# Optimization experiments

Hardware: AMD Instinct MI355X
Metric: run time of the kernel (lower is better)

## Reference

```python
import jax, jax.numpy as jnp
import numpy as np
from math import sqrt

N, D = 8192, 64

def setup_inputs() -> dict:
    key = jax.random.key(0)
    kq, kk, kv = jax.random.split(key, 3)
    q = jax.random.normal(kq, (N, D), dtype=jnp.float32)
    k = jax.random.normal(kk, (N, D), dtype=jnp.float32)
    v = jax.random.normal(kv, (N, D), dtype=jnp.float32)
    return {"q": q, "k": k, "v": v}

def reference(q, k, v):
    # Mathematically identical to the block-wise online-softmax loop:
    # after processing all KV blocks, m_blk == rowmax(S), l_blk == rowsum(exp(S - m)),
    # O = (exp(S - m) @ V) / l.
    scale = 1.0 / sqrt(q.shape[-1])
    S = (q @ k.T) * scale            # [N, N] attention scores
    m = jnp.max(S, axis=1, keepdims=True)   # running max -> global row max
    P = jnp.exp(S - m)                      # unnormalized probs
    L = jnp.sum(P, axis=1, keepdims=True)   # softmax denominator, [N, 1]
    O = (P @ v) / L                          # [N, D]
    return (O, L)
```

## Files before the change

kernel.cpp:

```cpp
#include <hip/hip_runtime.h>
#include <hip/hip_bf16.h>
#include <math.h>

#define N 8192
#define D 64
#define QSCALE 0.18033688011112042f

typedef __attribute__((ext_vector_type(8))) short short8;
typedef __attribute__((ext_vector_type(16))) float f32x16;
typedef __attribute__((ext_vector_type(4))) unsigned int ui4;

__device__ inline short f32_to_bf16_bits(float x) {
    unsigned u = __builtin_bit_cast(unsigned, x);
    u += 0x7FFFu + ((u >> 16) & 1u);
    return (short)(u >> 16);
}
__device__ inline float bfbits_to_f32(unsigned short u) {
    return __builtin_bit_cast(float, ((unsigned)u) << 16);
}
__device__ inline unsigned cvt_pk_bf16(float a, float b) {
    unsigned r;
    asm("v_cvt_pk_bf16_f32 %0, %1, %2" : "=v"(r) : "v"(a), "v"(b));
    return r;
}
__device__ inline float max3f(float a, float b, float c) {
    float d;
    asm("v_max3_f32 %0, %1, %2, %3" : "=v"(d) : "v"(a), "v"(b), "v"(c));
    return d;
}

__global__ __launch_bounds__(256) void fa_conv(const float* __restrict__ q,
                                               const float* __restrict__ k,
                                               const float* __restrict__ v,
                                               short* __restrict__ Qb,
                                               short* __restrict__ Kp,
                                               short* __restrict__ Vp) {
    int bid = blockIdx.x, tid = threadIdx.x;
    if (bid < 512) {
        int i = (bid * 256 + tid) * 4;
        float4 a = *(const float4*)(q + i);
        unsigned lo = cvt_pk_bf16(a.x * QSCALE, a.y * QSCALE);
        unsigned hi = cvt_pk_bf16(a.z * QSCALE, a.w * QSCALE);
        unsigned long long u = (unsigned long long)lo | ((unsigned long long)hi << 32);
        *(unsigned long long*)(Qb + i) = u;
    } else if (bid < 768) {
        int t = bid - 512;
        int c = tid >> 6, l = tid & 63, ql = l & 31, hi = l >> 5;
        const float* src = k + (size_t)(t * 32 + ql) * D + c * 16 + hi * 8;
        float4 a = *(const float4*)(src);
        float4 b = *(const float4*)(src + 4);
        uint4 u = { cvt_pk_bf16(a.x, a.y), cvt_pk_bf16(a.z, a.w),
                    cvt_pk_bf16(b.x, b.y), cvt_pk_bf16(b.z, b.w) };
        *(uint4*)(Kp + (size_t)t * 2048 + c * 512 + l * 8) = u;
    } else {
        int t = bid - 768;
        int dt = tid >> 7, h = (tid >> 6) & 1, hi = (tid >> 5) & 1, ql = tid & 31;
        const float* src = v + (size_t)(t * 32 + h * 16 + hi * 4) * D + dt * 32 + ql;
        float f[8];
#pragma unroll
        for (int j = 0; j < 8; ++j)
            f[j] = src[(size_t)((j & 3) + 8 * (j >> 2)) * D];
        uint4 u = { cvt_pk_bf16(f[0], f[1]), cvt_pk_bf16(f[2], f[3]),
                    cvt_pk_bf16(f[4], f[5]), cvt_pk_bf16(f[6], f[7]) };
        *(uint4*)(Vp + (size_t)t * 2048 + dt * 1024 + h * 512 + hi * 256 + ql * 8) = u;
    }
}

__global__ __launch_bounds__(256) void fa_part_kernel(const short* __restrict__ Qb,
                                                      const short* __restrict__ Kp,
                                                      const short* __restrict__ Vp,
                                                      short* __restrict__ OTb,
                                                      float* __restrict__ Ml,
                                                      int KN) {
    const int s  = blockIdx.x & 15;
    const int qt = blockIdx.x >> 4;
    const int w = threadIdx.x >> 6, lane = threadIdx.x & 63;
    const int ql = lane & 31, hi = lane >> 5;
    const int qrow = qt * 128 + w * 32 + ql;

    const short* qp = Qb + (size_t)qrow * D + hi * 8;
    short8 qf0 = *(const short8*)(qp);
    short8 qf1 = *(const short8*)(qp + 16);
    short8 qf2 = *(const short8*)(qp + 32);
    short8 qf3 = *(const short8*)(qp + 48);

    f32x16 acc0 = {}, acc1 = {};
    float mex = -INFINITY, lsum = 0.f;

    const int t0 = (s * KN) >> 5, nt = KN >> 5;
    const short* kp = Kp + (size_t)t0 * 2048 + lane * 8;
    const short* vp = Vp + (size_t)t0 * 2048 + lane * 8;

    short8 kA0, kA1, kA2, kA3, kB0, kB1, kB2, kB3;
    short8 vA0, vA1, vA2, vA3, vB0, vB1, vB2, vB3;

#define LOADK(d0, d1, d2, d3) do {                                         \
        d0 = *(const short8*)(kp);                                         \
        d1 = *(const short8*)(kp + 512);                                   \
        d2 = *(const short8*)(kp + 1024);                                  \
        d3 = *(const short8*)(kp + 1536);                                  \
        kp += 2048;                                                        \
    } while (0)
#define LOADV(d0, d1, d2, d3) do {                                         \
        d0 = *(const short8*)(vp);                                         \
        d1 = *(const short8*)(vp + 512);                                   \
        d2 = *(const short8*)(vp + 1024);                                  \
        d3 = *(const short8*)(vp + 1536);                                  \
        vp += 2048;                                                        \
    } while (0)

#define TILE(K0, K1, K2, K3, V0, V1, V2, V3) do {                           \
        f32x16 st = {};                                                     \
        st = __builtin_amdgcn_mfma_f32_32x32x16_bf16(K0, qf0, st, 0, 0, 0); \
        st = __builtin_amdgcn_mfma_f32_32x32x16_bf16(K1, qf1, st, 0, 0, 0); \
        st = __builtin_amdgcn_mfma_f32_32x32x16_bf16(K2, qf2, st, 0, 0, 0); \
        st = __builtin_amdgcn_mfma_f32_32x32x16_bf16(K3, qf3, st, 0, 0, 0); \
        float m0_ = max3f(st[0], st[1], st[2]);                             \
        float m1_ = max3f(st[3], st[4], st[5]);                             \
        float m2_ = max3f(st[6], st[7], st[8]);                             \
        float m3_ = max3f(st[9], st[10], st[11]);                           \
        float m4_ = max3f(st[12], st[13], st[14]);                          \
        mex = max3f(mex, max3f(m0_, m1_, m2_), max3f(m3_, m4_, st[15]));    \
        unsigned pk0, pk1, pk2, pk3, pk4, pk5, pk6, pk7;                    \
        float rs_;                                                          \
        {                                                                   \
            float a_, b_;                                                   \
            a_ = __builtin_amdgcn_exp2f(st[0]);  b_ = __builtin_amdgcn_exp2f(st[1]);  \
            rs_ = a_ + b_;         pk0 = cvt_pk_bf16(a_, b_);               \
            a_ = __builtin_amdgcn_exp2f(st[2]);  b_ = __builtin_amdgcn_exp2f(st[3]);  \
            rs_ += a_ + b_;        pk1 = cvt_pk_bf16(a_, b_);               \
            a_ = __builtin_amdgcn_exp2f(st[4]);  b_ = __builtin_amdgcn_exp2f(st[5]);  \
            rs_ += a_ + b_;        pk2 = cvt_pk_bf16(a_, b_);               \
            a_ = __builtin_amdgcn_exp2f(st[6]);  b_ = __builtin_amdgcn_exp2f(st[7]);  \
            rs_ += a_ + b_;        pk3 = cvt_pk_bf16(a_, b_);               \
            a_ = __builtin_amdgcn_exp2f(st[8]);  b_ = __builtin_amdgcn_exp2f(st[9]);  \
            rs_ += a_ + b_;        pk4 = cvt_pk_bf16(a_, b_);               \
            a_ = __builtin_amdgcn_exp2f(st[10]); b_ = __builtin_amdgcn_exp2f(st[11]); \
            rs_ += a_ + b_;        pk5 = cvt_pk_bf16(a_, b_);               \
            a_ = __builtin_amdgcn_exp2f(st[12]); b_ = __builtin_amdgcn_exp2f(st[13]); \
            rs_ += a_ + b_;        pk6 = cvt_pk_bf16(a_, b_);               \
            a_ = __builtin_amdgcn_exp2f(st[14]); b_ = __builtin_amdgcn_exp2f(st[15]); \
            rs_ += a_ + b_;        pk7 = cvt_pk_bf16(a_, b_);               \
        }                                                                   \
        lsum += rs_;                                                        \
        ui4 va_ = { pk0, pk1, pk2, pk3 };                                   \
        ui4 vb_ = { pk4, pk5, pk6, pk7 };                                   \
        short8 pb0 = __builtin_bit_cast(short8, va_);                       \
        short8 pb1 = __builtin_bit_cast(short8, vb_);                       \
        acc0 = __builtin_amdgcn_mfma_f32_32x32x16_bf16(V0, pb0, acc0, 0, 0, 0); \
        acc0 = __builtin_amdgcn_mfma_f32_32x32x16_bf16(V1, pb1, acc0, 0, 0, 0); \
        acc1 = __builtin_amdgcn_mfma_f32_32x32x16_bf16(V2, pb0, acc1, 0, 0, 0); \
        acc1 = __builtin_amdgcn_mfma_f32_32x32x16_bf16(V3, pb1, acc1, 0, 0, 0); \
    } while (0)

    LOADK(kA0, kA1, kA2, kA3);
    LOADV(vA0, vA1, vA2, vA3);
#pragma unroll 1
    for (int T = 0; T < nt; T += 2) {
        LOADK(kB0, kB1, kB2, kB3);
        LOADV(vB0, vB1, vB2, vB3);
        TILE(kA0, kA1, kA2, kA3, vA0, vA1, vA2, vA3);
        if (T + 2 < nt) {
            LOADK(kA0, kA1, kA2, kA3);
            LOADV(vA0, vA1, vA2, vA3);
        }
        TILE(kB0, kB1, kB2, kB3, vB0, vB1, vB2, vB3);
    }
#undef LOADK
#undef LOADV
#undef TILE

    mex = fmaxf(mex, __shfl_xor(mex, 32));
    lsum += __shfl_xor(lsum, 32);

#pragma unroll
    for (int r = 0; r < 16; ++r) {
        int d0 = (r & 3) + 8 * (r >> 2) + 4 * hi;
        OTb[(size_t)(s * 64 + d0) * N + qrow]      = f32_to_bf16_bits(acc0[r]);
        OTb[(size_t)(s * 64 + 32 + d0) * N + qrow] = f32_to_bf16_bits(acc1[r]);
    }
    if (hi == 0) {
        Ml[(size_t)(s * 2 + 0) * N + qrow] = lsum;
        Ml[(size_t)(s * 2 + 1) * N + qrow] = mex;
    }
}

__global__ __launch_bounds__(256) void fa_comb_kernel(const short* __restrict__ OTb,
                                                      const float* __restrict__ Ml,
                                                      float* __restrict__ Out, int S) {
    const int qb = blockIdx.x >> 2, db4 = blockIdx.x & 3;
    const int row = threadIdx.x & 63, dd = threadIdx.x >> 6;
    const int grow = qb * 64 + row;
    const int d0 = db4 * 16 + dd * 4;

    float v0 = 0.f, v1 = 0.f, v2 = 0.f, v3 = 0.f;
    float L = 0.f, mg = -INFINITY;
    for (int s = 0; s < S; ++s) {
        size_t base = (size_t)(s * 64 + d0) * N + grow;
        v0 += bfbits_to_f32((unsigned short)OTb[base]);
        v1 += bfbits_to_f32((unsigned short)OTb[base + (size_t)N]);
        v2 += bfbits_to_f32((unsigned short)OTb[base + (size_t)2 * N]);
        v3 += bfbits_to_f32((unsigned short)OTb[base + (size_t)3 * N]);
        L  += Ml[(size_t)(s * 2 + 0) * N + grow];
        mg = fmaxf(mg, Ml[(size_t)(s * 2 + 1) * N + grow]);
    }
    float inv = 1.0f / L;
    float4 o = { v0 * inv, v1 * inv, v2 * inv, v3 * inv };
    *(float4*)(Out + (size_t)grow * D + d0) = o;
    if (db4 == 0 && dd == 0) Out[(size_t)N * D + grow] = exp2f(-mg) * L;
}

extern "C" void kernel_launch(void* const* d_in, const int* in_sizes, int n_in,
                              void* d_out, int out_size, void* d_ws, size_t ws_size,
                              hipStream_t stream) {
    const float* q = (const float*)d_in[0];
    const float* k = (const float*)d_in[1];
    const float* v = (const float*)d_in[2];
    float* out = (float*)d_out;

    short* Qb = (short*)d_ws;
    short* Kp = Qb + (size_t)N * D;
    short* Vp = Kp + (size_t)N * D;
    short* OTb = (short*)((char*)d_ws + 3 * 1048576);

    int S = 16;
    while (S > 1 &&
           3ull * 1048576 + (size_t)S * (64ull * N * 2) + (size_t)S * (2ull * N * 4) > ws_size)
        S >>= 1;
    float* Ml = (float*)(OTb + (size_t)S * 64 * N);
    int KN = N / S;

    fa_conv<<<1024, 256, 0, stream>>>(q, k, v, Qb, Kp, Vp);
    fa_part_kernel<<<64 * S, 256, 0, stream>>>(Qb, Kp, Vp, OTb, Ml, KN);
    fa_comb_kernel<<<(N / 64) * 4, 256, 0, stream>>>(OTb, Ml, out, S);
}
```

Baseline: 45.36 us.

## Fuse bf16 conversion into attention kernel, stage K/V in LDS, use 32 splits

```diff
diff --git a/kernel.cpp b/kernel.cpp
--- a/kernel.cpp
+++ b/kernel.cpp
@@ -5,6 +5,9 @@
 #define N 8192
 #define D 64
 #define QSCALE 0.18033688011112042f
+#define SPLITS 32
+#define KVS 256
+#define NT (KVS / 32)
 
 typedef __attribute__((ext_vector_type(8))) short short8;
 typedef __attribute__((ext_vector_type(16))) float f32x16;
@@ -29,67 +32,75 @@
     return d;
 }
 
-__global__ __launch_bounds__(256) void fa_conv(const float* __restrict__ q,
-                                               const float* __restrict__ k,
-                                               const float* __restrict__ v,
-                                               short* __restrict__ Qb,
-                                               short* __restrict__ Kp,
-                                               short* __restrict__ Vp) {
-    int bid = blockIdx.x, tid = threadIdx.x;
-    if (bid < 512) {
-        int i = (bid * 256 + tid) * 4;
-        float4 a = *(const float4*)(q + i);
-        unsigned lo = cvt_pk_bf16(a.x * QSCALE, a.y * QSCALE);
-        unsigned hi = cvt_pk_bf16(a.z * QSCALE, a.w * QSCALE);
-        unsigned long long u = (unsigned long long)lo | ((unsigned long long)hi << 32);
-        *(unsigned long long*)(Qb + i) = u;
-    } else if (bid < 768) {
-        int t = bid - 512;
-        int c = tid >> 6, l = tid & 63, ql = l & 31, hi = l >> 5;
-        const float* src = k + (size_t)(t * 32 + ql) * D + c * 16 + hi * 8;
-        float4 a = *(const float4*)(src);
-        float4 b = *(const float4*)(src + 4);
-        uint4 u = { cvt_pk_bf16(a.x, a.y), cvt_pk_bf16(a.z, a.w),
-                    cvt_pk_bf16(b.x, b.y), cvt_pk_bf16(b.z, b.w) };
-        *(uint4*)(Kp + (size_t)t * 2048 + c * 512 + l * 8) = u;
-    } else {
-        int t = bid - 768;
-        int dt = tid >> 7, h = (tid >> 6) & 1, hi = (tid >> 5) & 1, ql = tid & 31;
-        const float* src = v + (size_t)(t * 32 + h * 16 + hi * 4) * D + dt * 32 + ql;
-        float f[8];
-#pragma unroll
-        for (int j = 0; j < 8; ++j)
-            f[j] = src[(size_t)((j & 3) + 8 * (j >> 2)) * D];
-        uint4 u = { cvt_pk_bf16(f[0], f[1]), cvt_pk_bf16(f[2], f[3]),
-                    cvt_pk_bf16(f[4], f[5]), cvt_pk_bf16(f[6], f[7]) };
-        *(uint4*)(Vp + (size_t)t * 2048 + dt * 1024 + h * 512 + hi * 256 + ql * 8) = u;
-    }
-}
-
-__global__ __launch_bounds__(256) void fa_part_kernel(const short* __restrict__ Qb,
-                                                      const short* __restrict__ Kp,
-                                                      const short* __restrict__ Vp,
+__global__ __launch_bounds__(256) void fa_part_kernel(const float* __restrict__ q,
+                                                      const float* __restrict__ k,
+                                                      const float* __restrict__ v,
                                                       short* __restrict__ OTb,
-                                                      float* __restrict__ Ml,
-                                                      int KN) {
-    const int s  = blockIdx.x & 15;
-    const int qt = blockIdx.x >> 4;
-    const int w = threadIdx.x >> 6, lane = threadIdx.x & 63;
+                                                      float* __restrict__ Ml) {
+    __shared__ short Klds[KVS * D];
+    __shared__ short Vlds[KVS * D];
+
+    const int s  = blockIdx.x & 31;
+    const int qt = blockIdx.x >> 5;
+    const int tid = threadIdx.x;
+    const int w = tid >> 6, lane = tid & 63;
     const int ql = lane & 31, hi = lane >> 5;
     const int qrow = qt * 128 + w * 32 + ql;
-
-    const short* qp = Qb + (size_t)qrow * D + hi * 8;
-    short8 qf0 = *(const short8*)(qp);
-    short8 qf1 = *(const short8*)(qp + 16);
-    short8 qf2 = *(const short8*)(qp + 32);
-    short8 qf3 = *(const short8*)(qp + 48);
+    const int k0 = s * KVS;
+
+    {
+        const int c = tid >> 6, l = tid & 63, kq = l & 31, kh = l >> 5;
+#pragma unroll
+        for (int t = 0; t < NT; ++t) {
+            const float* src = k + (size_t)(k0 + t * 32 + kq) * D + c * 16 + kh * 8;
+            float4 a = *(const float4*)(src);
+            float4 b = *(const float4*)(src + 4);
+            ui4 u = { cvt_pk_bf16(a.x, a.y), cvt_pk_bf16(a.z, a.w),
+                      cvt_pk_bf16(b.x, b.y), cvt_pk_bf16(b.z, b.w) };
+            *(ui4*)(Klds + t * 2048 + c * 512 + l * 8) = u;
+        }
+    }
+    {
+        const int dt = tid >> 7, h = (tid >> 6) & 1, h3 = (tid >> 5) & 1, vq = tid & 31;
+#pragma unroll
+        for (int t = 0; t < NT; ++t) {
+            const float* src = v + (size_t)(k0 + t * 32 + h * 16 + h3 * 4) * D + dt * 32 + vq;
+            float f[8];
+#pragma unroll
+            for (int j = 0; j < 8; ++j)
+                f[j] = src[(size_t)((j & 3) + 8 * (j >> 2)) * D];
+            ui4 u = { cvt_pk_bf16(f[0], f[1]), cvt_pk_bf16(f[2], f[3]),
+                      cvt_pk_bf16(f[4], f[5]), cvt_pk_bf16(f[6], f[7]) };
+            *(ui4*)(Vlds + t * 2048 + dt * 1024 + h * 512 + h3 * 256 + vq * 8) = u;
+        }
+    }
+
+    short8 qf0, qf1, qf2, qf3;
+    {
+        const float* qsrc = q + (size_t)qrow * D + hi * 8;
+#define QFRAG(dst, off) do {                                               \
+            float4 a = *(const float4*)(qsrc + (off));                     \
+            float4 b = *(const float4*)(qsrc + (off) + 4);                 \
+            ui4 u = { cvt_pk_bf16(a.x * QSCALE, a.y * QSCALE),             \
+                      cvt_pk_bf16(a.z * QSCALE, a.w * QSCALE),             \
+                      cvt_pk_bf16(b.x * QSCALE, b.y * QSCALE),             \
+                      cvt_pk_bf16(b.z * QSCALE, b.w * QSCALE) };           \
+            dst = __builtin_bit_cast(short8, u);                           \
+        } while (0)
+        QFRAG(qf0, 0);
+        QFRAG(qf1, 16);
+        QFRAG(qf2, 32);
+        QFRAG(qf3, 48);
+#undef QFRAG
+    }
+
+    __syncthreads();
 
     f32x16 acc0 = {}, acc1 = {};
     float mex = -INFINITY, lsum = 0.f;
 
-    const int t0 = (s * KN) >> 5, nt = KN >> 5;
-    const short* kp = Kp + (size_t)t0 * 2048 + lane * 8;
-    const short* vp = Vp + (size_t)t0 * 2048 + lane * 8;
+    const short* kp = Klds + lane * 8;
+    const short* vp = Vlds + lane * 8;
 
     short8 kA0, kA1, kA2, kA3, kB0, kB1, kB2, kB3;
     short8 vA0, vA1, vA2, vA3, vB0, vB1, vB2, vB3;
@@ -156,11 +167,11 @@
     LOADK(kA0, kA1, kA2, kA3);
     LOADV(vA0, vA1, vA2, vA3);
 #pragma unroll 1
-    for (int T = 0; T < nt; T += 2) {
+    for (int T = 0; T < NT; T += 2) {
         LOADK(kB0, kB1, kB2, kB3);
         LOADV(vB0, vB1, vB2, vB3);
         TILE(kA0, kA1, kA2, kA3, vA0, vA1, vA2, vA3);
-        if (T + 2 < nt) {
+        if (T + 2 < NT) {
             LOADK(kA0, kA1, kA2, kA3);
             LOADV(vA0, vA1, vA2, vA3);
         }
@@ -187,7 +198,7 @@
 
 __global__ __launch_bounds__(256) void fa_comb_kernel(const short* __restrict__ OTb,
                                                       const float* __restrict__ Ml,
-                                                      float* __restrict__ Out, int S) {
+                                                      float* __restrict__ Out) {
     const int qb = blockIdx.x >> 2, db4 = blockIdx.x & 3;
     const int row = threadIdx.x & 63, dd = threadIdx.x >> 6;
     const int grow = qb * 64 + row;
@@ -195,7 +206,7 @@
 
     float v0 = 0.f, v1 = 0.f, v2 = 0.f, v3 = 0.f;
     float L = 0.f, mg = -INFINITY;
-    for (int s = 0; s < S; ++s) {
+    for (int s = 0; s < SPLITS; ++s) {
         size_t base = (size_t)(s * 64 + d0) * N + grow;
         v0 += bfbits_to_f32((unsigned short)OTb[base]);
         v1 += bfbits_to_f32((unsigned short)OTb[base + (size_t)N]);
@@ -218,19 +229,9 @@
     const float* v = (const float*)d_in[2];
     float* out = (float*)d_out;
 
-    short* Qb = (short*)d_ws;
-    short* Kp = Qb + (size_t)N * D;
-    short* Vp = Kp + (size_t)N * D;
-    short* OTb = (short*)((char*)d_ws + 3 * 1048576);
-
-    int S = 16;
-    while (S > 1 &&
-           3ull * 1048576 + (size_t)S * (64ull * N * 2) + (size_t)S * (2ull * N * 4) > ws_size)
-        S >>= 1;
-    float* Ml = (float*)(OTb + (size_t)S * 64 * N);
-    int KN = N / S;
-
-    fa_conv<<<1024, 256, 0, stream>>>(q, k, v, Qb, Kp, Vp);
-    fa_part_kernel<<<64 * S, 256, 0, stream>>>(Qb, Kp, Vp, OTb, Ml, KN);
-    fa_comb_kernel<<<(N / 64) * 4, 256, 0, stream>>>(OTb, Ml, out, S);
-}
+    short* OTb = (short*)d_ws;
+    float* Ml = (float*)(OTb + (size_t)SPLITS * 64 * N);
+
+    fa_part_kernel<<<64 * SPLITS, 256, 0, stream>>>(q, k, v, OTb, Ml);
+    fa_comb_kernel<<<(N / 64) * 4, 256, 0, stream>>>(OTb, Ml, out);
+}
```

Result: slower. 49.32 us (+8.7%).
